# Kernel optimization log

Measured on AMD Instinct MI355X. Metric: run time of the kernel, lower is better.

Reference implementation:

```python
import jax, jax.numpy as jnp
import numpy as np

B, N, D = 2, 2048, 1024
H = 16
HD = D // H
C = 4
INTERACTION_BOOST = 0.3
EPS = 1e-6


def _rmsnorm(t, w):
    # t: (B,H,N,HD), w: (HD,)
    var = jnp.mean(t * t, axis=-1, keepdims=True)
    return t * jax.lax.rsqrt(var + EPS) * w


def setup_inputs() -> dict:
    key = jax.random.key(0)
    ks = jax.random.split(key, 8)
    return {
        "x": jax.random.normal(ks[0], (B, N, D), dtype=jnp.float32),
        "character_masks": jax.random.uniform(ks[1], (B, C, N), dtype=jnp.float32),
        "interaction_mask": jax.random.uniform(ks[2], (B, N, N), dtype=jnp.float32),
        "W_qkv": jax.random.normal(ks[3], (3 * D, D), dtype=jnp.float32) * 0.02,
        "W_out": jax.random.normal(ks[4], (D, D), dtype=jnp.float32) * 0.02,
        "q_norm_w": jnp.ones((HD,), dtype=jnp.float32),
        "k_norm_w": jnp.ones((HD,), dtype=jnp.float32),
        "isolation_gate": jax.random.uniform(ks[5], (H,), dtype=jnp.float32),
    }


def reference(x, character_masks, interaction_mask, W_qkv, W_out,
              q_norm_w, k_norm_w, isolation_gate) -> jnp.ndarray:
    b, n, d = x.shape
    h, hd = isolation_gate.shape[0], d // isolation_gate.shape[0]

    qkv = x @ W_qkv.T                       # (B,N,3D)
    q, k, v = jnp.split(qkv, 3, axis=-1)
    def to_heads(t):
        return t.reshape(b, n, h, hd).transpose(0, 2, 1, 3)  # (B,H,N,HD)
    q, k, v = to_heads(q), to_heads(k), to_heads(v)

    q = _rmsnorm(q, q_norm_w)
    k = _rmsnorm(k, k_norm_w)

    scale = hd ** -0.5
    attn = jnp.einsum('bhqd,bhkd->bhqk', q, k) * scale   # (B,H,N,N)

    # isolation bias: same-character co-membership, row-max normalized
    same = jnp.einsum('bcq,bck->bqk', character_masks, character_masks)  # (B,N,N)
    same = same / jnp.clip(jnp.max(same, axis=-1, keepdims=True), 1e-6)
    bias = (same - 0.5) * 2.0 + INTERACTION_BOOST * interaction_mask     # (B,N,N)

    gate = jnp.clip(isolation_gate, 0.0, 1.0)[None, :, None, None]       # (1,H,1,1)
    attn = attn + gate * bias[:, None, :, :] * 3.0

    attn = jax.nn.softmax(attn, axis=-1)
    out = jnp.einsum('bhqk,bhkd->bhqd', attn, v)          # (B,H,N,HD)
    out = out.transpose(0, 2, 1, 3).reshape(b, n, d)      # (B,N,D)
    return out @ W_out.T
```

## Files before the change

### kernel.cpp

```cpp
#include <hip/hip_runtime.h>
#include <math.h>


typedef __attribute__((ext_vector_type(8))) short s8v;
typedef __attribute__((ext_vector_type(4))) short s4v;
typedef __attribute__((ext_vector_type(4))) float f4v;

#define L2E 1.44269504088896340736f

__device__ __forceinline__ unsigned short f2bf(float x) {
    union { float f; unsigned u; } v; v.f = x;
    unsigned r = v.u + 0x7FFF + ((v.u >> 16) & 1);
    return (unsigned short)(r >> 16);
}
__device__ __forceinline__ float bf2f(unsigned short h) {
    union { unsigned u; float f; } v; v.u = ((unsigned)h) << 16;
    return v.f;
}
__device__ __forceinline__ f4v mfma32(s8v a, s8v b, f4v c) {
    return __builtin_amdgcn_mfma_f32_16x16x32_bf16(a, b, c, 0, 0, 0);
}
__device__ __forceinline__ f4v mfma16x16(s4v a, s4v b, f4v c) {
    return __builtin_amdgcn_mfma_f32_16x16x16bf16_1k(a, b, c, 0, 0, 0);
}
__device__ __forceinline__ void gl_lds16(const void* g, void* l) {
    __builtin_amdgcn_global_load_lds(
        (const __attribute__((address_space(1))) unsigned*)g,
        (__attribute__((address_space(3))) unsigned*)l, 16, 0, 0);
}
__device__ __forceinline__ float exp2g(float x) {
    float r; asm("v_exp_f32 %0, %1" : "=v"(r) : "v"(x)); return r;
}

__global__ __launch_bounds__(256)
void planes_k(const float* __restrict__ src, short* __restrict__ ph,
              short* __restrict__ pl)
{
    const int i = blockIdx.x * 256 + threadIdx.x;
    float4 f = ((const float4*)src)[i];
    float fa[4] = {f.x, f.y, f.z, f.w};
    s4v h4, l4;
#pragma unroll
    for (int j = 0; j < 4; j++) {
        unsigned short hb = f2bf(fa[j]);
        h4[j] = (short)hb;
        l4[j] = (short)f2bf(fa[j] - bf2f(hb));
    }
    ((s4v*)ph)[i] = h4;
    ((s4v*)pl)[i] = l4;
}

template<int MODE, int TM>
__global__ __launch_bounds__(256, 3)
void gemm_mfma(const short* __restrict__ Ah, const short* __restrict__ Al,
               const short* __restrict__ Bh, const short* __restrict__ Bl,
               short* __restrict__ Qhp, short* __restrict__ Qlp,
               short* __restrict__ Khp, short* __restrict__ Klp,
               short* __restrict__ Vp, float* __restrict__ Cout,
               const float* __restrict__ qw, const float* __restrict__ kw)
{
    constexpr int MJ = (TM == 128) ? 4 : 2;
    constexpr int JW = (TM == 128) ? 64 : 32;
    __shared__ short sAh[TM*32], sAl[TM*32], sBh[128*32], sBl[128*32];

    const int t = threadIdx.x, w = t >> 6, lane = t & 63;
    const int col = lane & 15, quad = lane >> 4;
    const int wm = (TM == 128) ? (w >> 1) : 0;
    const int wn = (TM == 128) ? (w & 1) : w;
    const int m0 = blockIdx.y * TM, n0 = blockIdx.x * 128;

    f4v acc[4][MJ];
#pragma unroll
    for (int i = 0; i < 4; i++)
#pragma unroll
        for (int j = 0; j < MJ; j++) { f4v z = {0.f,0.f,0.f,0.f}; acc[i][j] = z; }

    const int r4 = lane >> 2;
    const int cs = ((lane & 3) ^ (r4 & 3)) * 8;
    const short* agh = Ah + (size_t)(m0 + w*16 + r4)*1024 + cs;
    const short* agl = Al + (size_t)(m0 + w*16 + r4)*1024 + cs;
    const short* bgh = Bh + (size_t)(n0 + w*16 + r4)*1024 + cs;
    const short* bgl = Bl + (size_t)(n0 + w*16 + r4)*1024 + cs;

    for (int kt = 0; kt < 32; kt++) {
        const int k0 = kt * 32;
        __syncthreads();
#pragma unroll
        for (int j = 0; j < TM/64; j++) {
            gl_lds16(agh + k0 + j*65536, &sAh[(j*4 + w)*512]);
            gl_lds16(agl + k0 + j*65536, &sAl[(j*4 + w)*512]);
        }
#pragma unroll
        for (int j = 0; j < 2; j++) {
            gl_lds16(bgh + k0 + j*65536, &sBh[(j*4 + w)*512]);
            gl_lds16(bgl + k0 + j*65536, &sBl[(j*4 + w)*512]);
        }
        __syncthreads();

        const int swz = ((quad ^ (col & 3)) << 3);
        s8v ahf[4], alf[4], bhf[MJ], blf[MJ];
#pragma unroll
        for (int i = 0; i < 4; i++) {
            const int aoff = (wm*64 + i*16 + col)*32 + swz;
            ahf[i] = *(const s8v*)&sAh[aoff];
            alf[i] = *(const s8v*)&sAl[aoff];
        }
#pragma unroll
        for (int j = 0; j < MJ; j++) {
            const int boff = (wn*JW + j*16 + col)*32 + swz;
            bhf[j] = *(const s8v*)&sBh[boff];
            blf[j] = *(const s8v*)&sBl[boff];
        }
#pragma unroll
        for (int i = 0; i < 4; i++)
#pragma unroll
        for (int j = 0; j < MJ; j++) {
            acc[i][j] = mfma32(ahf[i], bhf[j], acc[i][j]);
            acc[i][j] = mfma32(ahf[i], blf[j], acc[i][j]);
            acc[i][j] = mfma32(alf[i], bhf[j], acc[i][j]);
        }
    }

    if (MODE == 0) {
        const int whichW = (n0 + wn*64) >> 10;
        if (whichW < 2) {
            const float* nw = (whichW == 0) ? qw : kw;
            const float sfac = (whichW == 0) ? (0.125f * L2E) : 1.0f;
            float wj[4];
#pragma unroll
            for (int j = 0; j < 4; j++) wj[j] = nw[j*16 + col] * sfac;
#pragma unroll
            for (int i = 0; i < 4; i++)
#pragma unroll
            for (int r = 0; r < 4; r++) {
                float s2 = acc[i][0][r]*acc[i][0][r] + acc[i][1][r]*acc[i][1][r]
                         + acc[i][2][r]*acc[i][2][r] + acc[i][3][r]*acc[i][3][r];
                s2 += __shfl_xor(s2, 1);
                s2 += __shfl_xor(s2, 2);
                s2 += __shfl_xor(s2, 4);
                s2 += __shfl_xor(s2, 8);
                const float scn = rsqrtf(s2*(1.0f/64.0f) + 1e-6f);
#pragma unroll
                for (int j = 0; j < 4; j++) acc[i][j][r] *= scn*wj[j];
            }
        }
    }

    if (MODE == 0) {
#pragma unroll
        for (int i = 0; i < 4; i++)
#pragma unroll
        for (int j = 0; j < MJ; j++) {
            const int gcol = n0 + wn*JW + j*16 + col;
            const int which = gcol >> 10;
            const int hh = (gcol >> 6) & 15;
            const int hd = gcol & 63;
            const int grow0 = m0 + wm*64 + i*16 + quad*4;
            const int b = grow0 >> 11, nn0 = grow0 & 2047;
            if (which == 2) {
                s4v hv;
#pragma unroll
                for (int r = 0; r < 4; r++) hv[r] = (short)f2bf(acc[i][j][r]);
                *(s4v*)&Vp[((size_t)(b*16 + hh)*64 + hd)*2048 + nn0] = hv;
            } else {
                short* Hp = (which == 0) ? Qhp : Khp;
                short* Lp = (which == 0) ? Qlp : Klp;
                const size_t base = ((size_t)(b*16 + hh)*2048 + nn0)*64 + hd;
#pragma unroll
                for (int r = 0; r < 4; r++) {
                    const float v = acc[i][j][r];
                    const unsigned short hb = f2bf(v);
                    union { float f; unsigned u; } rr; rr.f = v - bf2f(hb);
                    Hp[base + (size_t)r*64] = (short)hb;
                    Lp[base + (size_t)r*64] = (short)(rr.u >> 16);
                }
            }
        }
    } else {
#pragma unroll
        for (int i = 0; i < 4; i++)
#pragma unroll
        for (int j = 0; j < MJ; j++) {
            const int gcol = n0 + wn*JW + j*16 + col;
#pragma unroll
            for (int r = 0; r < 4; r++) {
                const int grow = m0 + wm*64 + i*16 + quad*4 + r;
                Cout[(size_t)grow*1024 + gcol] = acc[i][j][r];
            }
        }
    }
}

__global__ __launch_bounds__(256)
void rowscale_k(const float* __restrict__ cm, float* __restrict__ rs)
{
    __shared__ float cms[4][2048];
    const int b  = blockIdx.x >> 5;
    const int qt = blockIdx.x & 31;
    const float* base = cm + (size_t)b * 4 * 2048;
    for (int i = threadIdx.x; i < 2048; i += 256) {
        cms[0][i] = base[i];
        cms[1][i] = base[2048 + i];
        cms[2][i] = base[4096 + i];
        cms[3][i] = base[6144 + i];
    }
    __syncthreads();
    const int q    = qt * 64 + (threadIdx.x >> 2);
    const int part = threadIdx.x & 3;
    const float a0 = cms[0][q], a1 = cms[1][q], a2 = cms[2][q], a3 = cms[3][q];
    float mx = 0.f;
    for (int i = 0; i < 512; i++) {
        const int k = part + 4 * i;
        float d = a0*cms[0][k] + a1*cms[1][k] + a2*cms[2][k] + a3*cms[3][k];
        mx = fmaxf(mx, d);
    }
    mx = fmaxf(mx, __shfl_xor(mx, 1));
    mx = fmaxf(mx, __shfl_xor(mx, 2));
    if (part == 0) rs[b * 2048 + q] = 1.0f / fmaxf(mx, 1e-6f);
}

__global__ __launch_bounds__(256)
void bias_pre(const float* __restrict__ cm, const float* __restrict__ im,
              const float* __restrict__ rs, float* __restrict__ Bias2)
{
    const int bid = blockIdx.x;
    const int qq = bid & 3;
    const int kt = (bid >> 2) & 31;
    const int b  = bid >> 7;

    __shared__ float cmk[4][64];
    const int t = threadIdx.x;
    const int k0 = kt * 64;
    cmk[t >> 6][t & 63] = cm[(size_t)b*8192 + (t >> 6)*2048 + k0 + (t & 63)];
    __syncthreads();

    const int klane = t & 15;
    const int qrow  = t >> 4;
    const int kk = k0 + klane*4;
    const int kg = kk >> 2;
    float ck[4][4];
#pragma unroll
    for (int c = 0; c < 4; c++)
#pragma unroll
        for (int j = 0; j < 4; j++) ck[c][j] = cmk[c][klane*4 + j];

    const float* cmb = cm + (size_t)b * 8192;
    const float kS = 3.0f * L2E;
    for (int it = 0; it < 32; it++) {
        const int q = qq*512 + it*16 + qrow;
        float4 imv = *(const float4*)(im + ((size_t)b*2048 + q)*2048 + kk);
        const float rsq = rs[b*2048 + q];
        const float c0 = cmb[q], c1 = cmb[2048+q], c2 = cmb[4096+q], c3 = cmb[6144+q];
        float o[4];
        float iv[4] = {imv.x, imv.y, imv.z, imv.w};
#pragma unroll
        for (int j = 0; j < 4; j++) {
            float same = c0*ck[0][j] + c1*ck[1][j] + c2*ck[2][j] + c3*ck[3][j];
            o[j] = ((same*rsq - 0.5f)*2.0f + 0.3f*iv[j]) * kS;
        }
        *(float4*)(Bias2 + (((size_t)b*512 + kg)*2048 + q)*4) =
            make_float4(o[0], o[1], o[2], o[3]);
    }
}

__global__ __launch_bounds__(256, 2)
void attn_mfma(const short* __restrict__ Qhp, const short* __restrict__ Qlp,
               const short* __restrict__ Khg, const short* __restrict__ Klg,
               const short* __restrict__ VtG, const float* __restrict__ Bias2,
               const float* __restrict__ gate, short* __restrict__ Oh,
               short* __restrict__ Ol)
{
    const int bid = blockIdx.x;
    const int h  = bid & 15;
    const int qt = (bid >> 4) & 15;
    const int b  = bid >> 8;

    __shared__ __align__(16) short Kbuf[2][2][64*64];
    __shared__ __align__(16) short Vbuf[2][64*64];

    const int t    = threadIdx.x;
    const int w    = t >> 6;
    const int lane = t & 63;
    const int col  = lane & 15;
    const int quad = lane >> 4;

    const size_t headoff = ((size_t)(b*16 + h)) * 2048 * 64;
    const int qb = qt*128 + w*32;

    s8v qfh[2][2], qfl[2][2];
#pragma unroll
    for (int n = 0; n < 2; n++)
#pragma unroll
    for (int c = 0; c < 2; c++) {
        const size_t off = headoff + (size_t)(qb + n*16 + col)*64 + c*32 + quad*8;
        qfh[n][c] = *(const s8v*)(Qhp + off);
        qfl[n][c] = *(const s8v*)(Qlp + off);
    }

    const float g = fminf(fmaxf(gate[h], 0.f), 1.f);

    float mi[2] = {-INFINITY, -INFINITY};
    float li[2] = {0.f, 0.f};
    f4v Oa[4][2];
#pragma unroll
    for (int dt = 0; dt < 4; dt++)
#pragma unroll
        for (int n = 0; n < 2; n++) { f4v z = {0.f,0.f,0.f,0.f}; Oa[dt][n] = z; }

    const short* ksrc_h = Khg + headoff + (size_t)(w*8 + (lane>>3))*64
                          + ((lane&7) ^ (lane>>3))*8;
    const short* ksrc_l = Klg + headoff + (size_t)(w*8 + (lane>>3))*64
                          + ((lane&7) ^ (lane>>3))*8;
    const short* vsrcT = VtG + headoff + (size_t)(w*8 + (lane>>3))*2048
                          + ((lane&7) ^ (lane>>3))*8;

    const float* bptr[2];
#pragma unroll
    for (int n = 0; n < 2; n++)
        bptr[n] = Bias2 + (((size_t)b*512 + quad)*2048 + qb + n*16 + col)*4;

    int vkoff[4];
#pragma unroll
    for (int s = 0; s < 4; s++)
        vkoff[s] = ((((s << 1) | (quad >> 1)) ^ (col & 7)) << 3) + ((quad & 1) << 2);

    auto dma = [&](int kbase, int pp) {
#pragma unroll
        for (int j = 0; j < 2; j++) {
            gl_lds16(ksrc_h + (size_t)kbase*64 + j*2048, &Kbuf[pp][0][(j*4 + w)*512]);
            gl_lds16(ksrc_l + (size_t)kbase*64 + j*2048, &Kbuf[pp][1][(j*4 + w)*512]);
        }
#pragma unroll
        for (int cc = 0; cc < 2; cc++)
            gl_lds16(vsrcT + (size_t)(kbase + cc*65536), &Vbuf[pp][cc*2048 + w*512]);
    };

    float4 biasA[4][2], biasB[4][2];

    dma(0, 0);
#pragma unroll
    for (int s = 0; s < 4; s++)
#pragma unroll
    for (int n = 0; n < 2; n++)
        biasA[s][n] = *(const float4*)(bptr[n] + (size_t)s*4*8192);
    __syncthreads();

    auto tile = [&](int kt, int pp, float4 (&BC)[4][2], float4 (&BN)[4][2]) {
        const int kbase = kt * 64;
        const bool pre = kt < 31;
        if (pre) {
            dma(kbase + 64, pp ^ 1);
#pragma unroll
            for (int s = 0; s < 4; s++)
#pragma unroll
            for (int n = 0; n < 2; n++)
                BN[s][n] = *(const float4*)(bptr[n] +
                    ((size_t)((kbase >> 2) + 16) + s*4)*8192);
        }

        f4v S[4][2];
#pragma unroll
        for (int s = 0; s < 4; s++)
#pragma unroll
            for (int n = 0; n < 2; n++) { f4v z = {0.f,0.f,0.f,0.f}; S[s][n] = z; }
#pragma unroll
        for (int s = 0; s < 4; s++)
#pragma unroll
        for (int c = 0; c < 2; c++) {
            const int koff = (s*16 + col)*64 + (((c*4 + quad) ^ (col & 7)) << 3);
            s8v kh = *(const s8v*)&Kbuf[pp][0][koff];
            s8v kl = *(const s8v*)&Kbuf[pp][1][koff];
#pragma unroll
            for (int n = 0; n < 2; n++) {
                S[s][n] = mfma32(kh, qfh[n][c], S[s][n]);
                S[s][n] = mfma32(kh, qfl[n][c], S[s][n]);
                S[s][n] = mfma32(kl, qfh[n][c], S[s][n]);
            }
        }

        s4v ph[2][4];
#pragma unroll
        for (int n = 0; n < 2; n++) {
            float sr[4][4];
            float rmax = -INFINITY;
#pragma unroll
            for (int s = 0; s < 4; s++) {
                const float bb[4] = {BC[s][n].x, BC[s][n].y, BC[s][n].z, BC[s][n].w};
#pragma unroll
                for (int r = 0; r < 4; r++) {
                    sr[s][r] = fmaf(bb[r], g, S[s][n][r]);
                    rmax = fmaxf(rmax, sr[s][r]);
                }
            }
            rmax = fmaxf(rmax, __shfl_xor(rmax, 16));
            rmax = fmaxf(rmax, __shfl_xor(rmax, 32));
            if (!__all(rmax <= mi[n] + 8.f)) {
                const float mnew = fmaxf(mi[n], rmax);
                const float alpha = exp2g(mi[n] - mnew);
#pragma unroll
                for (int dt = 0; dt < 4; dt++)
#pragma unroll
                    for (int r = 0; r < 4; r++) Oa[dt][n][r] *= alpha;
                li[n] *= alpha;
                mi[n] = mnew;
            }
            float rsum = 0.f;
#pragma unroll
            for (int s = 0; s < 4; s++) {
                const float p0 = exp2g(sr[s][0] - mi[n]);
                const float p1 = exp2g(sr[s][1] - mi[n]);
                const float p2 = exp2g(sr[s][2] - mi[n]);
                const float p3 = exp2g(sr[s][3] - mi[n]);
                unsigned u01, u23;
                asm("v_cvt_pk_bf16_f32 %0, %1, %2" : "=v"(u01) : "v"(p0), "v"(p1));
                asm("v_cvt_pk_bf16_f32 %0, %1, %2" : "=v"(u23) : "v"(p2), "v"(p3));
                union { unsigned u; float f; } a0, a1, a2, a3;
                a0.u = u01 << 16; a1.u = u01 & 0xffff0000u;
                a2.u = u23 << 16; a3.u = u23 & 0xffff0000u;
                rsum += (a0.f + a1.f) + (a2.f + a3.f);
                union { unsigned uu[2]; s4v v; } pk;
                pk.uu[0] = u01; pk.uu[1] = u23;
                ph[n][s] = pk.v;
            }
            rsum += __shfl_xor(rsum, 16);
            rsum += __shfl_xor(rsum, 32);
            li[n] += rsum;
        }

#pragma unroll
        for (int dt = 0; dt < 4; dt++) {
            const int vrow = (dt*16 + col)*64;
#pragma unroll
            for (int s = 0; s < 4; s++) {
                s4v vh = *(const s4v*)&Vbuf[pp][vrow + vkoff[s]];
#pragma unroll
                for (int n = 0; n < 2; n++)
                    Oa[dt][n] = mfma16x16(vh, ph[n][s], Oa[dt][n]);
            }
        }

        if (pre) __syncthreads();
    };

    for (int kt = 0; kt < 32; kt += 2) {
        tile(kt,     0, biasA, biasB);
        tile(kt + 1, 1, biasB, biasA);
    }

#pragma unroll
    for (int n = 0; n < 2; n++) {
        const float inv = 1.0f / li[n];
        const size_t row = (size_t)b*2048 + qb + n*16 + col;
#pragma unroll
        for (int dt = 0; dt < 4; dt++) {
            s4v hv, lv;
#pragma unroll
            for (int r = 0; r < 4; r++) {
                float y = Oa[dt][n][r] * inv;
                unsigned short hb = f2bf(y);
                hv[r] = (short)hb;
                union { float f; unsigned u; } rr; rr.f = y - bf2f(hb);
                lv[r] = (short)(rr.u >> 16);
            }
            const size_t o = row*1024 + h*64 + dt*16 + quad*4;
            *(s4v*)&Oh[o] = hv;
            *(s4v*)&Ol[o] = lv;
        }
    }
}

extern "C" void kernel_launch(void* const* d_in, const int* in_sizes, int n_in,
                              void* d_out, int out_size, void* d_ws, size_t ws_size,
                              hipStream_t stream)
{
    const float* x    = (const float*)d_in[0];
    const float* cm   = (const float*)d_in[1];
    const float* im   = (const float*)d_in[2];
    const float* Wqkv = (const float*)d_in[3];
    const float* Wout = (const float*)d_in[4];
    const float* qw   = (const float*)d_in[5];
    const float* kw   = (const float*)d_in[6];
    const float* gate = (const float*)d_in[7];
    float* out = (float*)d_out;

    char* ws = (char*)d_ws;
    short* qhp = (short*)(ws);
    short* qlp = (short*)(ws +  8388608);
    short* khp = (short*)(ws + 16777216);
    short* klp = (short*)(ws + 25165824);
    short* vp  = (short*)(ws + 33554432);
    short* oh  = (short*)(ws + 41943040);
    short* ol  = (short*)(ws + 50331648);
    short* woh = (short*)(ws + 58720256);
    short* wol = (short*)(ws + 60817408);
    float* rsb = (float*)(ws + 62914560);
    char*  U   = ws + 62930944;
    short* xh  = (short*)(U);
    short* xl  = (short*)(U +  8388608);
    short* wqh = (short*)(U + 16777216);
    short* wql = (short*)(U + 23068672);
    float* bias2 = (float*)(U);

    planes_k<<<4096, 256, 0, stream>>>(x,    xh,  xl);
    planes_k<<<3072, 256, 0, stream>>>(Wqkv, wqh, wql);
    planes_k<<<1024, 256, 0, stream>>>(Wout, woh, wol);
    gemm_mfma<0,128><<<dim3(24, 32), 256, 0, stream>>>(xh, xl, wqh, wql,
        qhp, qlp, khp, klp, vp, nullptr, qw, kw);
    rowscale_k<<<64, 256, 0, stream>>>(cm, rsb);
    bias_pre<<<256, 256, 0, stream>>>(cm, im, rsb, bias2);
    attn_mfma<<<512, 256, 0, stream>>>(qhp, qlp, khp, klp, vp, bias2, gate,
                                       oh, ol);
    gemm_mfma<1,64><<<dim3(8, 64), 256, 0, stream>>>(oh, ol, woh, wol,
        nullptr, nullptr, nullptr, nullptr, nullptr, out, nullptr, nullptr);
}
```

Before: 368.3 us.

## Use 16x16x32 MFMA for PV with permuted V layout and MFMA row sums

The QKV projection epilogue now stores V^T with a permuted sequence index within each 64-key block. This lets the attention kernel load 8-element V fragments and run the P·V product with the K=32 bf16 MFMA instead of twice as many K=16 MFMAs. The softmax row-sum is now computed by an MFMA against a ones vector rather than by scalar bf16 unpacking, adds and cross-lane shuffles. The aim is fewer LDS reads, fewer instructions and fewer shuffles in the inner loop. The cost is four extra MFMAs per tile and a coupled layout change that must match across both kernels.

```diff
diff --git a/kernel.cpp b/kernel.cpp
--- a/kernel.cpp
+++ b/kernel.cpp
@@ -19,9 +19,6 @@
 }
 __device__ __forceinline__ f4v mfma32(s8v a, s8v b, f4v c) {
     return __builtin_amdgcn_mfma_f32_16x16x32_bf16(a, b, c, 0, 0, 0);
-}
-__device__ __forceinline__ f4v mfma16x16(s4v a, s4v b, f4v c) {
-    return __builtin_amdgcn_mfma_f32_16x16x16bf16_1k(a, b, c, 0, 0, 0);
 }
 __device__ __forceinline__ void gl_lds16(const void* g, void* l) {
     __builtin_amdgcn_global_load_lds(
@@ -161,7 +158,8 @@
                 s4v hv;
 #pragma unroll
                 for (int r = 0; r < 4; r++) hv[r] = (short)f2bf(acc[i][j][r]);
-                *(s4v*)&Vp[((size_t)(b*16 + hh)*64 + hd)*2048 + nn0] = hv;
+                const int nswz = (nn0 & ~60) | ((nn0 & 12) << 2) | ((nn0 & 48) >> 2);
+                *(s4v*)&Vp[((size_t)(b*16 + hh)*64 + hd)*2048 + nswz] = hv;
             } else {
                 short* Hp = (which == 0) ? Qhp : Khp;
                 short* Lp = (which == 0) ? Qlp : Klp;
@@ -299,13 +297,21 @@
 
     const float g = fminf(fmaxf(gate[h], 0.f), 1.f);
 
+    s8v ones8;
+#pragma unroll
+    for (int j = 0; j < 8; j++) ones8[j] = (short)0x3F80;
+
     float mi[2] = {-INFINITY, -INFINITY};
-    float li[2] = {0.f, 0.f};
+    f4v liacc[2];
     f4v Oa[4][2];
-#pragma unroll
-    for (int dt = 0; dt < 4; dt++)
-#pragma unroll
-        for (int n = 0; n < 2; n++) { f4v z = {0.f,0.f,0.f,0.f}; Oa[dt][n] = z; }
+    {
+        f4v z = {0.f,0.f,0.f,0.f};
+        liacc[0] = z; liacc[1] = z;
+#pragma unroll
+        for (int dt = 0; dt < 4; dt++)
+#pragma unroll
+            for (int n = 0; n < 2; n++) Oa[dt][n] = z;
+    }
 
     const short* ksrc_h = Khg + headoff + (size_t)(w*8 + (lane>>3))*64
                           + ((lane&7) ^ (lane>>3))*8;
@@ -319,11 +325,6 @@
     for (int n = 0; n < 2; n++)
         bptr[n] = Bias2 + (((size_t)b*512 + quad)*2048 + qb + n*16 + col)*4;
 
-    int vkoff[4];
-#pragma unroll
-    for (int s = 0; s < 4; s++)
-        vkoff[s] = ((((s << 1) | (quad >> 1)) ^ (col & 7)) << 3) + ((quad & 1) << 2);
-
     auto dma = [&](int kbase, int pp) {
 #pragma unroll
         for (int j = 0; j < 2; j++) {
@@ -378,20 +379,23 @@
             }
         }
 
-        s4v ph[2][4];
+        s8v ph8[2][2];
 #pragma unroll
         for (int n = 0; n < 2; n++) {
             float sr[4][4];
-            float rmax = -INFINITY;
 #pragma unroll
             for (int s = 0; s < 4; s++) {
                 const float bb[4] = {BC[s][n].x, BC[s][n].y, BC[s][n].z, BC[s][n].w};
 #pragma unroll
-                for (int r = 0; r < 4; r++) {
+                for (int r = 0; r < 4; r++)
                     sr[s][r] = fmaf(bb[r], g, S[s][n][r]);
-                    rmax = fmaxf(rmax, sr[s][r]);
-                }
-            }
+            }
+            float mx[4];
+#pragma unroll
+            for (int s = 0; s < 4; s++)
+                mx[s] = fmaxf(fmaxf(sr[s][0], sr[s][1]),
+                              fmaxf(sr[s][2], sr[s][3]));
+            float rmax = fmaxf(fmaxf(mx[0], mx[1]), fmaxf(mx[2], mx[3]));
             rmax = fmaxf(rmax, __shfl_xor(rmax, 16));
             rmax = fmaxf(rmax, __shfl_xor(rmax, 32));
             if (!__all(rmax <= mi[n] + 8.f)) {
@@ -401,10 +405,10 @@
                 for (int dt = 0; dt < 4; dt++)
 #pragma unroll
                     for (int r = 0; r < 4; r++) Oa[dt][n][r] *= alpha;
-                li[n] *= alpha;
+                liacc[n][0] *= alpha;
                 mi[n] = mnew;
             }
-            float rsum = 0.f;
+            union { unsigned uu[4]; s8v v; } pk0, pk1;
 #pragma unroll
             for (int s = 0; s < 4; s++) {
                 const float p0 = exp2g(sr[s][0] - mi[n]);
@@ -414,28 +418,28 @@
                 unsigned u01, u23;
                 asm("v_cvt_pk_bf16_f32 %0, %1, %2" : "=v"(u01) : "v"(p0), "v"(p1));
                 asm("v_cvt_pk_bf16_f32 %0, %1, %2" : "=v"(u23) : "v"(p2), "v"(p3));
-                union { unsigned u; float f; } a0, a1, a2, a3;
-                a0.u = u01 << 16; a1.u = u01 & 0xffff0000u;
-                a2.u = u23 << 16; a3.u = u23 & 0xffff0000u;
-                rsum += (a0.f + a1.f) + (a2.f + a3.f);
-                union { unsigned uu[2]; s4v v; } pk;
-                pk.uu[0] = u01; pk.uu[1] = u23;
-                ph[n][s] = pk.v;
-            }
-            rsum += __shfl_xor(rsum, 16);
-            rsum += __shfl_xor(rsum, 32);
-            li[n] += rsum;
-        }
+                if (s < 2) { pk0.uu[s*2] = u01;     pk0.uu[s*2 + 1] = u23; }
+                else       { pk1.uu[(s-2)*2] = u01; pk1.uu[(s-2)*2 + 1] = u23; }
+            }
+            ph8[n][0] = pk0.v;
+            ph8[n][1] = pk1.v;
+        }
+
+#pragma unroll
+        for (int n = 0; n < 2; n++)
+#pragma unroll
+        for (int m = 0; m < 2; m++)
+            liacc[n] = mfma32(ones8, ph8[n][m], liacc[n]);
 
 #pragma unroll
         for (int dt = 0; dt < 4; dt++) {
             const int vrow = (dt*16 + col)*64;
-#pragma unroll
-            for (int s = 0; s < 4; s++) {
-                s4v vh = *(const s4v*)&Vbuf[pp][vrow + vkoff[s]];
-#pragma unroll
-                for (int n = 0; n < 2; n++)
-                    Oa[dt][n] = mfma16x16(vh, ph[n][s], Oa[dt][n]);
+            s8v v0 = *(const s8v*)&Vbuf[pp][vrow + ((((quad*2)    ) ^ (col & 7)) << 3)];
+            s8v v1 = *(const s8v*)&Vbuf[pp][vrow + ((((quad*2) + 1) ^ (col & 7)) << 3)];
+#pragma unroll
+            for (int n = 0; n < 2; n++) {
+                Oa[dt][n] = mfma32(v0, ph8[n][0], Oa[dt][n]);
+                Oa[dt][n] = mfma32(v1, ph8[n][1], Oa[dt][n]);
             }
         }
 
@@ -449,7 +453,7 @@
 
 #pragma unroll
     for (int n = 0; n < 2; n++) {
-        const float inv = 1.0f / li[n];
+        const float inv = 1.0f / liacc[n][0];
         const size_t row = (size_t)b*2048 + qb + n*16 + col;
 #pragma unroll
         for (int dt = 0; dt < 4; dt++) {
```

Result: no change. 361.6 us (-1.8%).
